# Optimization experiments

Hardware: AMD Instinct MI355X
Metric: run time of the kernel (lower is better)

## Reference

```python
import math
import jax, jax.numpy as jnp
import numpy as np

B, T, C, H = 2, 2048, 1024, 16
HD = C // H

def gelu_tanh(x):
    # 0.5*x*(1+tanh(sqrt(2/pi)*(x+0.044715*x^3)))
    c = math.sqrt(2.0 / math.pi)
    return 0.5 * x * (1.0 + jnp.tanh(c * (x + 0.044715 * x * x * x)))

def layernorm(x, g, b, eps=1e-5):
    mu = jnp.mean(x, axis=-1, keepdims=True)
    var = jnp.var(x, axis=-1, keepdims=True)
    return (x - mu) * jax.lax.rsqrt(var + eps) * g + b

def setup_inputs() -> dict:
    key = jax.random.key(0)
    ks = jax.random.split(key, 6)
    s = 0.02
    return {
        "x": jax.random.normal(ks[0], (B, T, C), jnp.float32),
        "ln1_g": jnp.ones((C,), jnp.float32),
        "ln1_b": jnp.zeros((C,), jnp.float32),
        "W_qkv": jax.random.normal(ks[1], (C, 3 * C), jnp.float32) * s,
        "b_qkv": jnp.zeros((3 * C,), jnp.float32),
        "W_out": jax.random.normal(ks[2], (C, C), jnp.float32) * s,
        "b_out": jnp.zeros((C,), jnp.float32),
        "ln2_g": jnp.ones((C,), jnp.float32),
        "ln2_b": jnp.zeros((C,), jnp.float32),
        "W_fc1": jax.random.normal(ks[3], (C, 4 * C), jnp.float32) * s,
        "b_fc1": jnp.zeros((4 * C,), jnp.float32),
        "W_fc2": jax.random.normal(ks[4], (4 * C, C), jnp.float32) * s,
        "b_fc2": jnp.zeros((C,), jnp.float32),
    }

def reference(x, ln1_g, ln1_b, W_qkv, b_qkv, W_out, b_out,
              ln2_g, ln2_b, W_fc1, b_fc1, W_fc2, b_fc2):
    # pre-LN causal self-attention
    h = layernorm(x, ln1_g, ln1_b)
    qkv = h @ W_qkv + b_qkv                      # [B,T,3C]
    q, k, v = jnp.split(qkv, 3, axis=-1)
    q = q.reshape(B, T, H, HD).transpose(0, 2, 1, 3)  # [B,H,T,HD]
    k = k.reshape(B, T, H, HD).transpose(0, 2, 1, 3)
    v = v.reshape(B, T, H, HD).transpose(0, 2, 1, 3)
    scores = jnp.einsum("bhqd,bhkd->bhqk", q, k) * (1.0 / math.sqrt(HD))
    causal = jnp.tril(jnp.ones((T, T), bool))
    scores = jnp.where(causal, scores, jnp.float32(-jnp.inf))
    att = jax.nn.softmax(scores, axis=-1)
    out = jnp.einsum("bhqk,bhkd->bhqd", att, v)  # [B,H,T,HD]
    out = out.transpose(0, 2, 1, 3).reshape(B, T, C)
    out = out @ W_out + b_out
    temp = x + out
    # GELU MLP
    h2 = layernorm(temp, ln2_g, ln2_b)
    ff = gelu_tanh(h2 @ W_fc1 + b_fc1) @ W_fc2 + b_fc2
    return temp + ff
```

## Files before the change

kernel.cpp:

```cpp
#include <hip/hip_runtime.h>
#include <stdint.h>

#define Bb 2
#define Tt 2048
#define Cc 1024
#define Hh 16
#define HD 64
#define Mm (Bb*Tt)

typedef __bf16 bf16x8 __attribute__((ext_vector_type(8)));
typedef float  f32x4  __attribute__((ext_vector_type(4)));

#define DEV static __device__ __forceinline__

DEV float asfloat_(uint32_t u){ union{uint32_t u; float f;} x; x.u=u; return x.f; }
DEV uint32_t asuint_(float f){ union{float f; uint32_t u;} x; x.f=f; return x.u; }
DEV unsigned short f2bf(float f){
  uint32_t u = asuint_(f);
  uint32_t r = (u + 0x7fffu + ((u>>16)&1u)) >> 16;
  return (unsigned short)r;
}
DEV float gelu_(float x){
  float x3 = x*x*x;
  float t  = 0.7978845608028654f * (x + 0.044715f*x3);
  float e  = __expf(2.0f*t);
  float th = 1.0f - 2.0f/(e + 1.0f);
  return 0.5f * x * (1.0f + th);
}

#define GLL(gsrc, ldst) __builtin_amdgcn_global_load_lds( \
    (const __attribute__((address_space(1))) void*)(gsrc), \
    (__attribute__((address_space(3))) void*)(ldst), 16, 0, 0)

__global__ void wcvt_kernel(const float* __restrict__ W, unsigned short* __restrict__ WT,
                            int K, int N) {
  __shared__ float tile[32][33];
  int tx = threadIdx.x & 31, ty = threadIdx.x >> 5;
  int kb = blockIdx.x * 32, nb = blockIdx.y * 32;
  #pragma unroll
  for (int r = 0; r < 32; r += 8)
    tile[ty + r][tx] = W[(size_t)(kb + ty + r) * N + nb + tx];
  __syncthreads();
  #pragma unroll
  for (int r = 0; r < 32; r += 8)
    WT[(size_t)(nb + ty + r) * K + kb + tx] = f2bf(tile[tx][ty + r]);
}

__global__ void ln_kernel(const float* __restrict__ X, const float* __restrict__ g,
                          const float* __restrict__ bb, unsigned short* __restrict__ O) {
  int row = blockIdx.x, t = threadIdx.x;
  const float4* xr = (const float4*)(X + (size_t)row * Cc);
  float4 v = xr[t];
  float s = v.x + v.y + v.z + v.w;
  float q = v.x*v.x + v.y*v.y + v.z*v.z + v.w*v.w;
  #pragma unroll
  for (int o = 32; o > 0; o >>= 1) { s += __shfl_xor(s, o); q += __shfl_xor(q, o); }
  __shared__ float ss[4], sq[4];
  int w = t >> 6;
  if ((t & 63) == 0) { ss[w] = s; sq[w] = q; }
  __syncthreads();
  s = ss[0] + ss[1] + ss[2] + ss[3];
  q = sq[0] + sq[1] + sq[2] + sq[3];
  float mu  = s * (1.0f/Cc);
  float var = q * (1.0f/Cc) - mu*mu;
  float rstd = rsqrtf(var + 1e-5f);
  float4 gv = ((const float4*)g)[t], bv = ((const float4*)bb)[t];
  ushort4 o4;
  o4.x = f2bf((v.x-mu)*rstd*gv.x + bv.x);
  o4.y = f2bf((v.y-mu)*rstd*gv.y + bv.y);
  o4.z = f2bf((v.z-mu)*rstd*gv.z + bv.z);
  o4.w = f2bf((v.w-mu)*rstd*gv.w + bv.w);
  ((ushort4*)(O + (size_t)row * Cc))[t] = o4;
}

template<int MODE>
__launch_bounds__(512, 4)
__global__ void gemm_kernel(const unsigned short* __restrict__ A,
                            const unsigned short* __restrict__ BT,
                            const float* __restrict__ bias,
                            const float* __restrict__ res,
                            void* __restrict__ Cout,
                            int N, int K) {
  __shared__ unsigned short As[2][128*64];
  __shared__ unsigned short Bs[2][128*64];
  int tid  = threadIdx.x;
  int lane = tid & 63, w = tid >> 6;
  int wr = w >> 2, wc = w & 3;
  int g = lane >> 4, ql = lane & 15;
  int bm = blockIdx.x, bn = blockIdx.y;

  f32x4 acc[4][2];
  #pragma unroll
  for (int m = 0; m < 4; ++m)
    #pragma unroll
    for (int n = 0; n < 2; ++n) acc[m][n] = (f32x4){0.f,0.f,0.f,0.f};

  int r  = tid >> 3;
  int cc = tid & 7;
  int sc = (cc ^ (r & 7)) * 8;
  const unsigned short* Ag = A  + (size_t)(bm*128 + r) * K + sc;
  const unsigned short* Bg = BT + (size_t)(bn*128 + r) * K + sc;
  int sw = (ql & 7) << 3;
  int nk = K >> 6;

  GLL(Ag,                 As[0] + w*512);
  GLL(Ag + (size_t)64*K,  As[0] + 4096 + w*512);
  GLL(Bg,                 Bs[0] + w*512);
  GLL(Bg + (size_t)64*K,  Bs[0] + 4096 + w*512);
  __syncthreads();

  int cur = 0;
  for (int kt = 0; kt < nk; ++kt) {
    if (kt + 1 < nk) {
      const unsigned short* ag = Ag + (kt+1)*64;
      const unsigned short* bg = Bg + (kt+1)*64;
      GLL(ag,                 As[cur^1] + w*512);
      GLL(ag + (size_t)64*K,  As[cur^1] + 4096 + w*512);
      GLL(bg,                 Bs[cur^1] + w*512);
      GLL(bg + (size_t)64*K,  Bs[cur^1] + 4096 + w*512);
    }
    const unsigned short* Asc = As[cur];
    const unsigned short* Bsc = Bs[cur];
    #pragma unroll
    for (int kk = 0; kk < 2; ++kk) {
      int col = (kk*32 + g*8) ^ sw;
      bf16x8 af[4], bf2[2];
      #pragma unroll
      for (int m = 0; m < 4; ++m)
        af[m] = *(const bf16x8*)(Asc + (wr*64 + m*16 + ql)*64 + col);
      #pragma unroll
      for (int n = 0; n < 2; ++n)
        bf2[n] = *(const bf16x8*)(Bsc + (wc*32 + n*16 + ql)*64 + col);
      #pragma unroll
      for (int m = 0; m < 4; ++m)
        #pragma unroll
        for (int n = 0; n < 2; ++n)
          acc[m][n] = __builtin_amdgcn_mfma_f32_16x16x32_bf16(af[m], bf2[n], acc[m][n], 0, 0, 0);
    }
    __syncthreads();
    cur ^= 1;
  }

  int r0 = bm*128 + wr*64;
  int c0 = bn*128 + wc*32;
  int lr = g * 4;
  #pragma unroll
  for (int m = 0; m < 4; ++m) {
    #pragma unroll
    for (int n = 0; n < 2; ++n) {
      int col = c0 + n*16 + ql;
      float bv = bias[col];
      #pragma unroll
      for (int i = 0; i < 4; ++i) {
        int row = r0 + m*16 + lr + i;
        float v = acc[m][n][i] + bv;
        if (MODE == 2) v = gelu_(v);
        ((unsigned short*)Cout)[(size_t)row * N + col] = f2bf(v);
      }
    }
  }
}

__launch_bounds__(1024, 2)
__global__ void gemm_skrf_kernel(const unsigned short* __restrict__ A,
                                 const unsigned short* __restrict__ BT,
                                 const float* __restrict__ bias,
                                 const float* __restrict__ res,
                                 float* __restrict__ Cout,
                                 int N, int K) {
  __shared__ __align__(16) unsigned short SMEM[2][32768];
  int tid  = threadIdx.x;
  int lane = tid & 63, w = tid >> 6;
  int wg = w >> 3, w8 = w & 7;
  int wr = w8 >> 2, wc = w8 & 3;
  int g = lane >> 4, ql = lane & 15;
  int bm = blockIdx.x, bn = blockIdx.y;

  f32x4 acc[4][2];
  #pragma unroll
  for (int m = 0; m < 4; ++m)
    #pragma unroll
    for (int n = 0; n < 2; ++n) acc[m][n] = (f32x4){0.f,0.f,0.f,0.f};

  int tid_h = tid & 511;
  int r  = tid_h >> 3;
  int cc = tid_h & 7;
  int sc = (cc ^ (r & 7)) * 8;
  int kbase = wg * (K >> 1);
  const unsigned short* Ag = A  + (size_t)(bm*128 + r) * K + kbase + sc;
  const unsigned short* Bg = BT + (size_t)(bn*128 + r) * K + kbase + sc;
  int sw = (ql & 7) << 3;
  int nk = K >> 7;

  GLL(Ag,                 SMEM[0] + wg*8192 + w8*512);
  GLL(Ag + (size_t)64*K,  SMEM[0] + wg*8192 + 4096 + w8*512);
  GLL(Bg,                 SMEM[0] + 16384 + wg*8192 + w8*512);
  GLL(Bg + (size_t)64*K,  SMEM[0] + 16384 + wg*8192 + 4096 + w8*512);
  __syncthreads();

  int cur = 0;
  for (int kt = 0; kt < nk; ++kt) {
    if (kt + 1 < nk) {
      const unsigned short* ag = Ag + (kt+1)*64;
      const unsigned short* bg = Bg + (kt+1)*64;
      unsigned short* nb = SMEM[cur^1];
      GLL(ag,                 nb + wg*8192 + w8*512);
      GLL(ag + (size_t)64*K,  nb + wg*8192 + 4096 + w8*512);
      GLL(bg,                 nb + 16384 + wg*8192 + w8*512);
      GLL(bg + (size_t)64*K,  nb + 16384 + wg*8192 + 4096 + w8*512);
    }
    const unsigned short* AsH = SMEM[cur] + wg*8192;
    const unsigned short* BsH = SMEM[cur] + 16384 + wg*8192;
    #pragma unroll
    for (int kk = 0; kk < 2; ++kk) {
      int col = (kk*32 + g*8) ^ sw;
      bf16x8 af[4], bf2[2];
      #pragma unroll
      for (int m = 0; m < 4; ++m)
        af[m] = *(const bf16x8*)(AsH + (wr*64 + m*16 + ql)*64 + col);
      #pragma unroll
      for (int n = 0; n < 2; ++n)
        bf2[n] = *(const bf16x8*)(BsH + (wc*32 + n*16 + ql)*64 + col);
      #pragma unroll
      for (int m = 0; m < 4; ++m)
        #pragma unroll
        for (int n = 0; n < 2; ++n)
          acc[m][n] = __builtin_amdgcn_mfma_f32_16x16x32_bf16(af[m], bf2[n], acc[m][n], 0, 0, 0);
    }
    __syncthreads();
    cur ^= 1;
  }

  float* ex = (float*)SMEM[0];
  int eb = (w8*64 + lane) * 32;
  if (wg == 1) {
    #pragma unroll
    for (int m = 0; m < 4; ++m)
      #pragma unroll
      for (int n = 0; n < 2; ++n) {
        int c = m*2 + n;
        *(f32x4*)&ex[eb + ((c ^ (lane & 7)) << 2)] = acc[m][n];
      }
  }
  __syncthreads();
  if (wg == 0) {
    #pragma unroll
    for (int m = 0; m < 4; ++m)
      #pragma unroll
      for (int n = 0; n < 2; ++n) {
        int c = m*2 + n;
        f32x4 o = *(const f32x4*)&ex[eb + ((c ^ (lane & 7)) << 2)];
        acc[m][n][0] += o[0]; acc[m][n][1] += o[1];
        acc[m][n][2] += o[2]; acc[m][n][3] += o[3];
      }
    int r0 = bm*128 + wr*64;
    int c0 = bn*128 + wc*32;
    int lr = g * 4;
    #pragma unroll
    for (int m = 0; m < 4; ++m) {
      #pragma unroll
      for (int n = 0; n < 2; ++n) {
        int col = c0 + n*16 + ql;
        float bv = bias[col];
        #pragma unroll
        for (int i = 0; i < 4; ++i) {
          int row = r0 + m*16 + lr + i;
          Cout[(size_t)row * N + col] = acc[m][n][i] + bv + res[(size_t)row * N + col];
        }
      }
    }
  }
}

__global__ void vtr_kernel(const unsigned short* __restrict__ qkv,
                           unsigned short* __restrict__ vtb) {
  __shared__ unsigned short Tl[64][72];
  int tid = threadIdx.x;
  int bh = blockIdx.x, tc = blockIdx.y;
  int b = bh >> 4, h = bh & 15;
  int r = tid >> 2, c0 = (tid & 3) * 16;
  const unsigned short* src = qkv + (size_t)(b*Tt + tc*64 + r)*3072 + 2048 + h*64 + c0;
  *(int4*)&Tl[r][c0]     = *(const int4*)(src);
  *(int4*)&Tl[r][c0 + 8] = *(const int4*)(src + 8);
  __syncthreads();
  int d = tid >> 2, k0 = (tid & 3) * 16;
  ushort4 o[4];
  #pragma unroll
  for (int jj = 0; jj < 4; ++jj) {
    o[jj].x = Tl[k0 + jj*4 + 0][d];
    o[jj].y = Tl[k0 + jj*4 + 1][d];
    o[jj].z = Tl[k0 + jj*4 + 2][d];
    o[jj].w = Tl[k0 + jj*4 + 3][d];
  }
  unsigned short* dst = vtb + ((size_t)(bh*64 + d))*2048 + tc*64 + k0;
  *(int4*)(dst)     = *(int4*)&o[0];
  *(int4*)(dst + 8) = *(int4*)&o[2];
}

__global__ __launch_bounds__(512, 4)
void attn_kernel(const unsigned short* __restrict__ qkv,
                 const unsigned short* __restrict__ vtb,
                 unsigned short* __restrict__ att) {
  __shared__ __align__(16) char smem[36864];
  int tid  = threadIdx.x;
  int lane = tid & 63, w = tid >> 6;
  int g = lane >> 4, ql = lane & 15;

  int bid = blockIdx.x;
  int bh = bid & 31;
  int jj = bid >> 5;
  int j  = (jj < 8) ? (2*jj) : (31 - 2*jj);
  int b = bh >> 4, h = bh & 15;
  int Q0 = j * 128;
  int qbase = Q0 + w * 16;
  char* Pb = smem + 16384 + w * 2560;

  const unsigned short* qrow = qkv + (size_t)(b*Tt + qbase + ql) * 3072 + h*64;
  bf16x8 qf0 = *(const bf16x8*)(qrow + g*8);
  bf16x8 qf1 = *(const bf16x8*)(qrow + 32 + g*8);

  f32x4 O[4];
  #pragma unroll
  for (int d = 0; d < 4; ++d) O[d] = (f32x4){0.f,0.f,0.f,0.f};
  float mrun = -1e30f, lrun = 0.f;

  int nt = Q0/64 + 2;

  int srow = tid >> 3;
  int scol = (tid & 7) * 8;
  int wr_off = srow*128 + ((scol*2) ^ ((srow & 7) << 4));
  const unsigned short* Kg = qkv + (size_t)(b*Tt + srow)*3072 + 1024 + h*64 + scol;
  const unsigned short* Vg = vtb + ((size_t)(bh*64 + srow))*2048 + scol;

  int4 kreg = *(const int4*)(Kg);
  int4 vreg = *(const int4*)(Vg);

  for (int t0 = 0; t0 < nt; ++t0) {
    __syncthreads();
    *(int4*)(smem + wr_off)        = kreg;
    *(int4*)(smem + 8192 + wr_off) = vreg;
    __syncthreads();
    if (t0 + 1 < nt) {
      kreg = *(const int4*)(Kg + (size_t)(t0+1)*64*3072);
      vreg = *(const int4*)(Vg + (t0+1)*64);
    }
    if (t0*64 > qbase + 15) continue;

    bool full = (t0*64 + 63) <= qbase;
    float ps[16];
    #pragma unroll
    for (int s = 0; s < 4; ++s) {
      int krow = s*16 + ql;
      int kb0 = krow*128 + (( g*16      ) ^ ((krow&7)<<4));
      int kb1 = krow*128 + (( g*16 + 64 ) ^ ((krow&7)<<4));
      bf16x8 kf0 = *(const bf16x8*)(smem + kb0);
      bf16x8 kf1 = *(const bf16x8*)(smem + kb1);
      f32x4 a = (f32x4){0.f,0.f,0.f,0.f};
      a = __builtin_amdgcn_mfma_f32_16x16x32_bf16(kf0, qf0, a, 0, 0, 0);
      a = __builtin_amdgcn_mfma_f32_16x16x32_bf16(kf1, qf1, a, 0, 0, 0);
      #pragma unroll
      for (int i = 0; i < 4; ++i) ps[s*4+i] = a[i] * 0.125f;
    }
    if (!full) {
      #pragma unroll
      for (int s = 0; s < 4; ++s)
        #pragma unroll
        for (int i = 0; i < 4; ++i)
          if (t0*64 + s*16 + g*4 + i > qbase + ql) ps[s*4+i] = -1e30f;
    }
    float tm = ps[0];
    #pragma unroll
    for (int i = 1; i < 16; ++i) tm = fmaxf(tm, ps[i]);
    tm = fmaxf(tm, __shfl_xor(tm, 16));
    tm = fmaxf(tm, __shfl_xor(tm, 32));
    float mnew = fmaxf(mrun, tm);
    float corr = __expf(mrun - mnew);
    float tsum = 0.f;
    #pragma unroll
    for (int s = 0; s < 4; ++s) {
      float e0 = __expf(ps[s*4+0] - mnew);
      float e1 = __expf(ps[s*4+1] - mnew);
      float e2 = __expf(ps[s*4+2] - mnew);
      float e3 = __expf(ps[s*4+3] - mnew);
      tsum += (e0 + e1) + (e2 + e3);
      ushort4 pk;
      pk.x = f2bf(e0); pk.y = f2bf(e1); pk.z = f2bf(e2); pk.w = f2bf(e3);
      *(ushort4*)(Pb + ql*160 + s*32 + g*8) = pk;
    }
    tsum += __shfl_xor(tsum, 16);
    tsum += __shfl_xor(tsum, 32);
    lrun = lrun * corr + tsum;
    mrun = mnew;

    float c0 = __shfl(corr, g*4 + 0);
    float c1 = __shfl(corr, g*4 + 1);
    float c2 = __shfl(corr, g*4 + 2);
    float c3 = __shfl(corr, g*4 + 3);
    #pragma unroll
    for (int d = 0; d < 4; ++d) {
      O[d][0] *= c0; O[d][1] *= c1; O[d][2] *= c2; O[d][3] *= c3;
    }
    #pragma unroll
    for (int kk = 0; kk < 2; ++kk) {
      bf16x8 pf = *(const bf16x8*)(Pb + ql*160 + kk*64 + g*16);
      #pragma unroll
      for (int d = 0; d < 4; ++d) {
        int drow = d*16 + ql;
        int vb = drow*128 + ((kk*64 + g*16) ^ ((drow&7)<<4));
        bf16x8 vf = *(const bf16x8*)(smem + 8192 + vb);
        O[d] = __builtin_amdgcn_mfma_f32_16x16x32_bf16(pf, vf, O[d], 0, 0, 0);
      }
    }
  }

  float l0 = __shfl(lrun, g*4 + 0);
  float l1 = __shfl(lrun, g*4 + 1);
  float l2 = __shfl(lrun, g*4 + 2);
  float l3 = __shfl(lrun, g*4 + 3);
  #pragma unroll
  for (int d = 0; d < 4; ++d) {
    size_t base = (size_t)(b*Tt + qbase)*Cc + h*64 + d*16 + ql;
    att[base + (size_t)(g*4+0)*Cc] = f2bf(O[d][0] / l0);
    att[base + (size_t)(g*4+1)*Cc] = f2bf(O[d][1] / l1);
    att[base + (size_t)(g*4+2)*Cc] = f2bf(O[d][2] / l2);
    att[base + (size_t)(g*4+3)*Cc] = f2bf(O[d][3] / l3);
  }
}

extern "C" void kernel_launch(void* const* d_in, const int* in_sizes, int n_in,
                              void* d_out, int out_size, void* d_ws, size_t ws_size,
                              hipStream_t stream) {
  const float* x    = (const float*)d_in[0];
  const float* ln1g = (const float*)d_in[1];
  const float* ln1b = (const float*)d_in[2];
  const float* Wqkv = (const float*)d_in[3];
  const float* bqkv = (const float*)d_in[4];
  const float* Wout = (const float*)d_in[5];
  const float* bout = (const float*)d_in[6];
  const float* ln2g = (const float*)d_in[7];
  const float* ln2b = (const float*)d_in[8];
  const float* Wfc1 = (const float*)d_in[9];
  const float* bfc1 = (const float*)d_in[10];
  const float* Wfc2 = (const float*)d_in[11];
  const float* bfc2 = (const float*)d_in[12];

  char* ws = (char*)d_ws;
  unsigned short* wqkvT = (unsigned short*)(ws);
  unsigned short* woutT = (unsigned short*)(ws + (6u<<20));
  unsigned short* wfc1T = (unsigned short*)(ws + (8u<<20));
  unsigned short* wfc2T = (unsigned short*)(ws + (16u<<20));
  unsigned short* vtb   = (unsigned short*)(ws + (24u<<20));
  float*          temp  = (float*)(ws + (24u<<20));
  unsigned short* hbuf  = (unsigned short*)(ws + (40u<<20));
  unsigned short* qkvb  = (unsigned short*)(ws + (48u<<20));
  unsigned short* attb  = (unsigned short*)(ws + (72u<<20));
  unsigned short* a1b   = (unsigned short*)(ws + (48u<<20));

  dim3 b256(256), b512(512), b1024(1024);
  wcvt_kernel<<<dim3(1024/32, 3072/32), b256, 0, stream>>>(Wqkv, wqkvT, 1024, 3072);
  wcvt_kernel<<<dim3(1024/32, 1024/32), b256, 0, stream>>>(Wout, woutT, 1024, 1024);
  wcvt_kernel<<<dim3(1024/32, 4096/32), b256, 0, stream>>>(Wfc1, wfc1T, 1024, 4096);
  wcvt_kernel<<<dim3(4096/32, 1024/32), b256, 0, stream>>>(Wfc2, wfc2T, 4096, 1024);

  ln_kernel<<<Mm, b256, 0, stream>>>(x, ln1g, ln1b, hbuf);
  gemm_kernel<0><<<dim3(Mm/128, 3072/128), b512, 0, stream>>>(hbuf, wqkvT, bqkv, nullptr, qkvb, 3072, 1024);
  vtr_kernel<<<dim3(32, 32), b256, 0, stream>>>(qkvb, vtb);
  attn_kernel<<<dim3(512), 512, 0, stream>>>(qkvb, vtb, attb);
  gemm_skrf_kernel<<<dim3(Mm/128, 1024/128), b1024, 0, stream>>>(attb, woutT, bout, x, temp, 1024, 1024);
  ln_kernel<<<Mm, b256, 0, stream>>>(temp, ln2g, ln2b, hbuf);
  gemm_kernel<2><<<dim3(Mm/128, 4096/128), b512, 0, stream>>>(hbuf, wfc1T, bfc1, nullptr, a1b, 4096, 1024);
  gemm_skrf_kernel<<<dim3(Mm/128, 1024/128), b1024, 0, stream>>>(a1b, wfc2T, bfc2, temp, (float*)d_out, 1024, 4096);
}
```

Baseline: 323.4 us.

## Triple-buffer GEMM LDS tiles with two-stage prefetch and explicit vmcnt waits

Turns the GEMM main loop's double-buffered LDS staging into a three-stage ring that prefetches two K-tiles ahead. It replaces __syncthreads with explicit s_waitcnt vmcnt plus s_barrier and a sched_barrier, so one tile's global loads can stay in flight while the current tile is consumed. LDS use grows from 64KB to 96KB per block and launch bounds drop from 4 to 2 blocks per CU, which lowers occupancy in exchange for deeper latency hiding.

```diff
diff --git a/kernel.cpp b/kernel.cpp
--- a/kernel.cpp
+++ b/kernel.cpp
@@ -74,15 +74,15 @@
 }
 
 template<int MODE>
-__launch_bounds__(512, 4)
+__launch_bounds__(512, 2)
 __global__ void gemm_kernel(const unsigned short* __restrict__ A,
                             const unsigned short* __restrict__ BT,
                             const float* __restrict__ bias,
                             const float* __restrict__ res,
                             void* __restrict__ Cout,
                             int N, int K) {
-  __shared__ unsigned short As[2][128*64];
-  __shared__ unsigned short Bs[2][128*64];
+  __shared__ unsigned short As[3][128*64];
+  __shared__ unsigned short Bs[3][128*64];
   int tid  = threadIdx.x;
   int lane = tid & 63, w = tid >> 6;
   int wr = w >> 2, wc = w & 3;
@@ -103,42 +103,56 @@
   int sw = (ql & 7) << 3;
   int nk = K >> 6;
 
-  GLL(Ag,                 As[0] + w*512);
-  GLL(Ag + (size_t)64*K,  As[0] + 4096 + w*512);
-  GLL(Bg,                 Bs[0] + w*512);
-  GLL(Bg + (size_t)64*K,  Bs[0] + 4096 + w*512);
-  __syncthreads();
-
-  int cur = 0;
+  GLL(Ag,                      As[0] + w*512);
+  GLL(Ag + (size_t)64*K,       As[0] + 4096 + w*512);
+  GLL(Bg,                      Bs[0] + w*512);
+  GLL(Bg + (size_t)64*K,       Bs[0] + 4096 + w*512);
+  GLL(Ag + 64,                 As[1] + w*512);
+  GLL(Ag + (size_t)64*K + 64,  As[1] + 4096 + w*512);
+  GLL(Bg + 64,                 Bs[1] + w*512);
+  GLL(Bg + (size_t)64*K + 64,  Bs[1] + 4096 + w*512);
+  asm volatile("s_waitcnt vmcnt(4)" ::: "memory");
+  __builtin_amdgcn_s_barrier();
+  __builtin_amdgcn_sched_barrier(0);
+
+  unsigned short *a0 = As[0], *a1 = As[1], *a2 = As[2];
+  unsigned short *b0 = Bs[0], *b1 = Bs[1], *b2 = Bs[2];
+
   for (int kt = 0; kt < nk; ++kt) {
-    if (kt + 1 < nk) {
-      const unsigned short* ag = Ag + (kt+1)*64;
-      const unsigned short* bg = Bg + (kt+1)*64;
-      GLL(ag,                 As[cur^1] + w*512);
-      GLL(ag + (size_t)64*K,  As[cur^1] + 4096 + w*512);
-      GLL(bg,                 Bs[cur^1] + w*512);
-      GLL(bg + (size_t)64*K,  Bs[cur^1] + 4096 + w*512);
-    }
-    const unsigned short* Asc = As[cur];
-    const unsigned short* Bsc = Bs[cur];
+    if (kt + 2 < nk) {
+      const unsigned short* ag = Ag + (kt+2)*64;
+      const unsigned short* bg = Bg + (kt+2)*64;
+      GLL(ag,                 a2 + w*512);
+      GLL(ag + (size_t)64*K,  a2 + 4096 + w*512);
+      GLL(bg,                 b2 + w*512);
+      GLL(bg + (size_t)64*K,  b2 + 4096 + w*512);
+    }
     #pragma unroll
     for (int kk = 0; kk < 2; ++kk) {
       int col = (kk*32 + g*8) ^ sw;
       bf16x8 af[4], bf2[2];
       #pragma unroll
       for (int m = 0; m < 4; ++m)
-        af[m] = *(const bf16x8*)(Asc + (wr*64 + m*16 + ql)*64 + col);
+        af[m] = *(const bf16x8*)(a0 + (wr*64 + m*16 + ql)*64 + col);
       #pragma unroll
       for (int n = 0; n < 2; ++n)
-        bf2[n] = *(const bf16x8*)(Bsc + (wc*32 + n*16 + ql)*64 + col);
+        bf2[n] = *(const bf16x8*)(b0 + (wc*32 + n*16 + ql)*64 + col);
       #pragma unroll
       for (int m = 0; m < 4; ++m)
         #pragma unroll
         for (int n = 0; n < 2; ++n)
           acc[m][n] = __builtin_amdgcn_mfma_f32_16x16x32_bf16(af[m], bf2[n], acc[m][n], 0, 0, 0);
     }
-    __syncthreads();
-    cur ^= 1;
+    if (kt + 2 < nk) {
+      asm volatile("s_waitcnt vmcnt(4)" ::: "memory");
+    } else if (kt + 1 < nk) {
+      asm volatile("s_waitcnt vmcnt(0)" ::: "memory");
+    }
+    __builtin_amdgcn_s_barrier();
+    __builtin_amdgcn_sched_barrier(0);
+    unsigned short* t;
+    t = a0; a0 = a1; a1 = a2; a2 = t;
+    t = b0; b0 = b1; b1 = b2; b2 = t;
   }
 
   int r0 = bm*128 + wr*64;
```

After: 373.4 us. +15.5%, slower.

## Add XCD-aware block swizzle and single-buffer LDS in GEMM

Applied to the files above, without the earlier changes.

Flattens the GEMM grids to 1D and remaps block ids so consecutive tiles land on the same XCD, meant to improve L2 reuse of A/B tiles. The main GEMM also drops its double-buffered LDS prefetch for a single buffer with load-sync-compute steps. That halves shared memory, which may allow more resident blocks, but removes the overlap of global loads with MFMA work. The unused residual parameter is removed from the main GEMM.

```diff
diff --git a/kernel.cpp b/kernel.cpp
--- a/kernel.cpp
+++ b/kernel.cpp
@@ -31,6 +31,11 @@
 #define GLL(gsrc, ldst) __builtin_amdgcn_global_load_lds( \
     (const __attribute__((address_space(1))) void*)(gsrc), \
     (__attribute__((address_space(3))) void*)(ldst), 16, 0, 0)
+
+DEV int xcd_swz(int p, int nwg) {
+  int cpx = nwg >> 3;
+  return (p & 7) * cpx + (p >> 3);
+}
 
 __global__ void wcvt_kernel(const float* __restrict__ W, unsigned short* __restrict__ WT,
                             int K, int N) {
@@ -78,16 +83,17 @@
 __global__ void gemm_kernel(const unsigned short* __restrict__ A,
                             const unsigned short* __restrict__ BT,
                             const float* __restrict__ bias,
-                            const float* __restrict__ res,
                             void* __restrict__ Cout,
                             int N, int K) {
-  __shared__ unsigned short As[2][128*64];
-  __shared__ unsigned short Bs[2][128*64];
+  __shared__ unsigned short As[128*64];
+  __shared__ unsigned short Bs[128*64];
   int tid  = threadIdx.x;
   int lane = tid & 63, w = tid >> 6;
   int wr = w >> 2, wc = w & 3;
   int g = lane >> 4, ql = lane & 15;
-  int bm = blockIdx.x, bn = blockIdx.y;
+  int nbn = N >> 7;
+  int lid = xcd_swz(blockIdx.x, gridDim.x);
+  int bm = lid / nbn, bn = lid % nbn;
 
   f32x4 acc[4][2];
   #pragma unroll
@@ -103,42 +109,32 @@
   int sw = (ql & 7) << 3;
   int nk = K >> 6;
 
-  GLL(Ag,                 As[0] + w*512);
-  GLL(Ag + (size_t)64*K,  As[0] + 4096 + w*512);
-  GLL(Bg,                 Bs[0] + w*512);
-  GLL(Bg + (size_t)64*K,  Bs[0] + 4096 + w*512);
-  __syncthreads();
-
-  int cur = 0;
   for (int kt = 0; kt < nk; ++kt) {
-    if (kt + 1 < nk) {
-      const unsigned short* ag = Ag + (kt+1)*64;
-      const unsigned short* bg = Bg + (kt+1)*64;
-      GLL(ag,                 As[cur^1] + w*512);
-      GLL(ag + (size_t)64*K,  As[cur^1] + 4096 + w*512);
-      GLL(bg,                 Bs[cur^1] + w*512);
-      GLL(bg + (size_t)64*K,  Bs[cur^1] + 4096 + w*512);
-    }
-    const unsigned short* Asc = As[cur];
-    const unsigned short* Bsc = Bs[cur];
+    if (kt) __syncthreads();
+    const unsigned short* ag = Ag + kt*64;
+    const unsigned short* bg = Bg + kt*64;
+    GLL(ag,                  As + w*512);
+    GLL(ag + (size_t)64*K,   As + 4096 + w*512);
+    GLL(bg,                  Bs + w*512);
+    GLL(bg + (size_t)64*K,   Bs + 4096 + w*512);
+    __syncthreads();
+
     #pragma unroll
     for (int kk = 0; kk < 2; ++kk) {
       int col = (kk*32 + g*8) ^ sw;
       bf16x8 af[4], bf2[2];
       #pragma unroll
       for (int m = 0; m < 4; ++m)
-        af[m] = *(const bf16x8*)(Asc + (wr*64 + m*16 + ql)*64 + col);
+        af[m] = *(const bf16x8*)(As + (wr*64 + m*16 + ql)*64 + col);
       #pragma unroll
       for (int n = 0; n < 2; ++n)
-        bf2[n] = *(const bf16x8*)(Bsc + (wc*32 + n*16 + ql)*64 + col);
+        bf2[n] = *(const bf16x8*)(Bs + (wc*32 + n*16 + ql)*64 + col);
       #pragma unroll
       for (int m = 0; m < 4; ++m)
         #pragma unroll
         for (int n = 0; n < 2; ++n)
           acc[m][n] = __builtin_amdgcn_mfma_f32_16x16x32_bf16(af[m], bf2[n], acc[m][n], 0, 0, 0);
     }
-    __syncthreads();
-    cur ^= 1;
   }
 
   int r0 = bm*128 + wr*64;
@@ -174,7 +170,9 @@
   int wg = w >> 3, w8 = w & 7;
   int wr = w8 >> 2, wc = w8 & 3;
   int g = lane >> 4, ql = lane & 15;
-  int bm = blockIdx.x, bn = blockIdx.y;
+  int nbn = N >> 7;
+  int lid = xcd_swz(blockIdx.x, gridDim.x);
+  int bm = lid / nbn, bn = lid % nbn;
 
   f32x4 acc[4][2];
   #pragma unroll
@@ -463,11 +461,11 @@
   wcvt_kernel<<<dim3(4096/32, 1024/32), b256, 0, stream>>>(Wfc2, wfc2T, 4096, 1024);
 
   ln_kernel<<<Mm, b256, 0, stream>>>(x, ln1g, ln1b, hbuf);
-  gemm_kernel<0><<<dim3(Mm/128, 3072/128), b512, 0, stream>>>(hbuf, wqkvT, bqkv, nullptr, qkvb, 3072, 1024);
+  gemm_kernel<0><<<dim3((Mm/128)*(3072/128)), b512, 0, stream>>>(hbuf, wqkvT, bqkv, qkvb, 3072, 1024);
   vtr_kernel<<<dim3(32, 32), b256, 0, stream>>>(qkvb, vtb);
   attn_kernel<<<dim3(512), 512, 0, stream>>>(qkvb, vtb, attb);
-  gemm_skrf_kernel<<<dim3(Mm/128, 1024/128), b1024, 0, stream>>>(attb, woutT, bout, x, temp, 1024, 1024);
+  gemm_skrf_kernel<<<dim3((Mm/128)*(1024/128)), b1024, 0, stream>>>(attb, woutT, bout, x, temp, 1024, 1024);
   ln_kernel<<<Mm, b256, 0, stream>>>(temp, ln2g, ln2b, hbuf);
-  gemm_kernel<2><<<dim3(Mm/128, 4096/128), b512, 0, stream>>>(hbuf, wfc1T, bfc1, nullptr, a1b, 4096, 1024);
-  gemm_skrf_kernel<<<dim3(Mm/128, 1024/128), b1024, 0, stream>>>(a1b, wfc2T, bfc2, temp, (float*)d_out, 1024, 4096);
-}
+  gemm_kernel<2><<<dim3((Mm/128)*(4096/128)), b512, 0, stream>>>(hbuf, wfc1T, bfc1, a1b, 4096, 1024);
+  gemm_skrf_kernel<<<dim3((Mm/128)*(1024/128)), b1024, 0, stream>>>(a1b, wfc2T, bfc2, temp, (float*)d_out, 1024, 4096);
+}
```

Result: slower. 331.0 us (+2.3%).
